# Kernel tuning notes

Measured on AMD Instinct MI355X. Metric: run time of the kernel, lower is better.

Reference implementation:

```python
import jax, jax.numpy as jnp
import numpy as np

B, T, C, L = 512, 256, 256, 64  # batch, time, num_classes (blank = C-1), max label len
NEG = -1e30  # log-space "zero"
EPS = 1e-7   # keras K.epsilon()


def setup_inputs() -> dict:
    key = jax.random.key(0)
    k1, k2, k3, k4 = jax.random.split(key, 4)
    # y_pred are post-softmax probabilities (output of the recognizer head)
    y_pred = jax.nn.softmax(jax.random.normal(k1, (B, T, C), jnp.float32), axis=-1)
    labels = jax.random.randint(k2, (B, L), 0, C - 1, dtype=jnp.int32)  # exclude blank
    input_length = jax.random.randint(k3, (B, 1), T // 2, T + 1, dtype=jnp.int32)
    label_length = jax.random.randint(k4, (B, 1), 16, 49, dtype=jnp.int32)
    return {"y_pred": y_pred, "labels": labels,
            "input_length": input_length, "label_length": label_length}


def _ctc_batch_cost(y_pred, labels, input_length, label_length):
    # Faithful to K.ctc_batch_cost: blank = num_classes-1, loss = -log p(labels | y_pred).
    Bn, Tn, Cn = y_pred.shape
    Ln = labels.shape[1]
    S = 2 * Ln + 1
    blank = Cn - 1
    log_probs = jnp.log(y_pred + EPS)                      # [B,T,C]

    # Extended label sequence: blank, l1, blank, l2, ..., blank  -> [B,S]
    ext = jnp.full((Bn, S), blank, dtype=labels.dtype)
    ext = ext.at[:, 1::2].set(labels)

    # Skip transition (s-2 -> s) allowed iff ext[s] != blank and ext[s] != ext[s-2]
    same2 = jnp.concatenate(
        [jnp.ones((Bn, 2), bool), ext[:, 2:] == ext[:, :-2]], axis=1)
    allow_skip = (ext != blank) & ~same2                   # [B,S]

    # Emission log-probs gathered along the extended sequence: [B,T,S]
    emit = jnp.take_along_axis(log_probs, jnp.broadcast_to(ext[:, None, :], (Bn, Tn, S)), axis=2)

    # alpha at t=0: can start at first blank or first label
    alpha0 = jnp.full((Bn, S), NEG, dtype=log_probs.dtype)
    alpha0 = alpha0.at[:, 0].set(emit[:, 0, 0])
    alpha0 = alpha0.at[:, 1].set(emit[:, 0, 1])

    def shift1(a):
        return jnp.concatenate([jnp.full((Bn, 1), NEG, a.dtype), a[:, :-1]], axis=1)

    def step(alpha, xs):
        emit_t, active = xs                                # [B,S], [B,1] bool
        a1 = shift1(alpha)
        a2 = shift1(a1)
        a2 = jnp.where(allow_skip, a2, NEG)
        new = jax.nn.logsumexp(jnp.stack([alpha, a1, a2]), axis=0) + emit_t
        new = jnp.where(active, new, alpha)                # freeze past input_length
        return new, None

    emits = jnp.transpose(emit, (1, 0, 2))[1:]             # [T-1,B,S]
    active = jnp.arange(1, Tn)[:, None, None] < input_length[None, :, :]  # [T-1,B,1]
    alpha_T, _ = jax.lax.scan(step, alpha0, (emits, active))

    # Terminal states: last label (s = 2*ll-1) or final blank (s = 2*ll)
    ll = label_length[:, 0]
    idx = jnp.stack([2 * ll - 1, 2 * ll], axis=1)          # [B,2]
    final = jnp.take_along_axis(alpha_T, idx, axis=1)
    return -jax.nn.logsumexp(final, axis=1, keepdims=True)  # [B,1]


def reference(y_pred, labels, input_length, label_length):
    return _ctc_batch_cost(y_pred, labels, input_length, label_length)
```

## Files before the change

### kernel.cpp

```cpp
#include <hip/hip_runtime.h>

#define TT 256
#define CC 256
#define LLAB 64
#define EPSF 1e-7f
#define CH 32
#define NSLOT 2
#define LN2F 0.69314718055994531f

__device__ __forceinline__ float wave_shr1_zero(float x) {
    int r = __builtin_amdgcn_update_dpp(0, __float_as_int(x), 0x138, 0xF, 0xF, false);
    return __int_as_float(r);
}

__device__ __forceinline__ float wave_max64(float x) {
#define DSTEP(ctrl)                                                            \
    { int t_ = __builtin_amdgcn_update_dpp(__float_as_int(x), __float_as_int(x),\
                                           (ctrl), 0xF, 0xF, false);           \
      x = fmaxf(x, __int_as_float(t_)); }
    DSTEP(0x111) DSTEP(0x112) DSTEP(0x114) DSTEP(0x118) DSTEP(0x142) DSTEP(0x143)
#undef DSTEP
    return __int_as_float(__builtin_amdgcn_readlane(__float_as_int(x), 63));
}

extern "C" __global__ __launch_bounds__(128) void ctc_fwd(
    const float* __restrict__ y_pred,
    const int* __restrict__ labels,
    const int* __restrict__ input_length,
    const int* __restrict__ label_length,
    float* __restrict__ out)
{
    const int b   = blockIdx.x;
    const int l   = threadIdx.x & 63;
    const int wid = threadIdx.x >> 6;

    __shared__ float lab_lds[NSLOT][CH][LLAB];
    __shared__ float blank_lds[NSLOT][CH];

    int len = input_length[b];
    len = len < 1 ? 1 : (len > TT ? TT : len);
    const int tmax = len - 1;
    const int nch  = (len - 1 + CH - 1) / CH;

    int llm = label_length[b];
    llm = llm < 1 ? 1 : (llm > LLAB ? LLAB : llm);

    const int  lab   = labels[b * LLAB + l];
    const bool ldlab = (l < llm);

    const float* __restrict__ yp = y_pred + (size_t)b * (TT * CC);
    const float* __restrict__ pl = yp + lab;
    const float* __restrict__ pb = yp + (CC - 1);

    float s0 = 0.f, s1 = 0.f, s2 = 0.f, skipf = 0.f;
    int   eacc = 0;

    float labA[CH], labB[CH], blA = 0.f, blB = 0.f;

#define ISSUE(c, labv, blv)                                                  \
    if ((c) < nch) {                                                         \
        const int t0 = 1 + (c) * CH;                                         \
        _Pragma("unroll")                                                    \
        for (int j = 0; j < CH; ++j) {                                       \
            int t = t0 + j; t = t > tmax ? tmax : t;                         \
            labv[j] = ldlab ? pl[t * CC] : 0.f;                              \
        }                                                                    \
        { int t = t0 + (l & (CH - 1)); t = t > tmax ? tmax : t;              \
          blv = pb[t * CC]; }                                                \
    }

#define FINISH(c, labv, blv)                                                 \
    if ((c) < nch) {                                                         \
        const int slot_ = (c) & (NSLOT - 1);                                 \
        if (l < CH) blank_lds[slot_][l] = blv + EPSF;                        \
        _Pragma("unroll")                                                    \
        for (int j = 0; j < CH; ++j)                                         \
            lab_lds[slot_][j][l] = ldlab ? (labv[j] + EPSF) : 0.f;           \
    }

    if (wid == 1) {
        ISSUE(0, labA, blA);
        ISSUE(1, labB, blB);
        FINISH(0, labA, blA);
    } else {
        const int labp = __shfl_up(lab, 1);
        skipf = (l >= 1 && lab != labp) ? 1.f : 0.f;
        if (l == 0) {
            s0 = pb[0] + EPSF;
            s1 = pl[0] + EPSF;
        }
    }
    __syncthreads();

    for (int k = 0; k < nch; ++k) {
        if (wid == 1) {
            if ((k & 1) == 0) { ISSUE(k + 2, labA, blA); FINISH(k + 1, labB, blB); }
            else              { ISSUE(k + 2, labB, blB); FINISH(k + 1, labA, blA); }
        } else {
            const int slot = k & (NSLOT - 1);
            float e[CH], bb[CH];
#pragma unroll
            for (int j = 0; j < CH; ++j) {
                e[j]  = lab_lds[slot][j][l];
                bb[j] = blank_lds[slot][j];
            }
#pragma unroll
            for (int j = 0; j < CH; ++j) {
                const int t = 1 + k * CH + j;
                float am1 = wave_shr1_zero(s1);
                float n0 = (s0 + am1) * bb[j];
                float n1 = fmaf(am1, skipf, s1 + s0) * e[j];
                float n2 = (s2 + s1) * bb[j];
                const bool act = t < len;
                s0 = act ? n0 : s0;
                s1 = act ? n1 : s1;
                s2 = act ? n2 : s2;
                if ((j & 3) == 3) {
                    float m = wave_max64(fmaxf(fmaxf(s0, s1), s2));
                    int me = __float_as_int(m) >> 23;
                    me = me < 26 ? 26 : me;
                    float scale = __int_as_float((253 - me) << 23);
                    s0 *= scale; s1 *= scale; s2 *= scale;
                    eacc += me - 126;
                }
            }
        }
        __syncthreads();
    }

    if (wid == 0) {
        float v1 = __shfl(s1, llm - 1);
        float v2 = (llm < LLAB) ? __shfl(s0, llm) : __shfl(s2, 63);
        float v  = fmaxf(v1 + v2, 1e-37f);
        if (l == 0) out[b] = -(__logf(v) + (float)eacc * LN2F);
    }
}

extern "C" void kernel_launch(void* const* d_in, const int* in_sizes, int n_in,
                              void* d_out, int out_size, void* d_ws, size_t ws_size,
                              hipStream_t stream) {
    (void)n_in; (void)out_size; (void)d_ws; (void)ws_size;
    const float* y_pred       = (const float*)d_in[0];
    const int*   labels       = (const int*)d_in[1];
    const int*   input_length = (const int*)d_in[2];
    const int*   label_length = (const int*)d_in[3];
    float* out = (float*)d_out;

    const int B = in_sizes[2];
    ctc_fwd<<<dim3(B), dim3(128), 0, stream>>>(y_pred, labels, input_length, label_length, out);
}
```

Measured before the change: 192.6 us.

## Load emissions directly into LDS via global_load_lds with manual vmcnt barriers

The producer wave now uses global_load_lds to stream the label and blank emission columns straight into a 4-slot LDS ring, instead of loading into registers and writing them to LDS. The EPS add and label masking move to the consumer wave. Each iteration waits with a hand-written vmcnt count and a raw s_barrier, replacing the two __syncthreads. This removes the register staging and the LDS store work from the producer and aims for deeper prefetch, but correctness depends on the hard-coded vmcnt(33) matching the 33 loads issued per chunk and on the slot reuse timing.

```diff
diff --git a/kernel.cpp b/kernel.cpp
--- a/kernel.cpp
+++ b/kernel.cpp
@@ -5,7 +5,7 @@
 #define LLAB 64
 #define EPSF 1e-7f
 #define CH 32
-#define NSLOT 2
+#define NSLOT 4
 #define LN2F 0.69314718055994531f
 
 __device__ __forceinline__ float wave_shr1_zero(float x) {
@@ -23,6 +23,12 @@
     return __int_as_float(__builtin_amdgcn_readlane(__float_as_int(x), 63));
 }
 
+__device__ __forceinline__ void gload_lds4(const float* g, float* lds) {
+    __builtin_amdgcn_global_load_lds(
+        (const __attribute__((address_space(1))) void*)g,
+        (__attribute__((address_space(3))) void*)lds, 4, 0, 0);
+}
+
 extern "C" __global__ __launch_bounds__(128) void ctc_fwd(
     const float* __restrict__ y_pred,
     const int* __restrict__ labels,
@@ -35,7 +41,7 @@
     const int wid = threadIdx.x >> 6;
 
     __shared__ float lab_lds[NSLOT][CH][LLAB];
-    __shared__ float blank_lds[NSLOT][CH];
+    __shared__ float blank_lds[NSLOT][LLAB];
 
     int len = input_length[b];
     len = len < 1 ? 1 : (len > TT ? TT : len);
@@ -51,37 +57,27 @@
     const float* __restrict__ yp = y_pred + (size_t)b * (TT * CC);
     const float* __restrict__ pl = yp + lab;
     const float* __restrict__ pb = yp + (CC - 1);
+    const float* __restrict__ psrc = ldlab ? pl : pb;
 
     float s0 = 0.f, s1 = 0.f, s2 = 0.f, skipf = 0.f;
     int   eacc = 0;
 
-    float labA[CH], labB[CH], blA = 0.f, blB = 0.f;
-
-#define ISSUE(c, labv, blv)                                                  \
+#define ISSUE_LDS(c)                                                         \
     if ((c) < nch) {                                                         \
+        const int slot_ = (c) & (NSLOT - 1);                                 \
         const int t0 = 1 + (c) * CH;                                         \
+        { int t = t0 + (l & (CH - 1)); t = t > tmax ? tmax : t;              \
+          gload_lds4(pb + t * CC, &blank_lds[slot_][0]); }                   \
         _Pragma("unroll")                                                    \
         for (int j = 0; j < CH; ++j) {                                       \
             int t = t0 + j; t = t > tmax ? tmax : t;                         \
-            labv[j] = ldlab ? pl[t * CC] : 0.f;                              \
+            gload_lds4(psrc + t * CC, &lab_lds[slot_][j][0]);                \
         }                                                                    \
-        { int t = t0 + (l & (CH - 1)); t = t > tmax ? tmax : t;              \
-          blv = pb[t * CC]; }                                                \
-    }
-
-#define FINISH(c, labv, blv)                                                 \
-    if ((c) < nch) {                                                         \
-        const int slot_ = (c) & (NSLOT - 1);                                 \
-        if (l < CH) blank_lds[slot_][l] = blv + EPSF;                        \
-        _Pragma("unroll")                                                    \
-        for (int j = 0; j < CH; ++j)                                         \
-            lab_lds[slot_][j][l] = ldlab ? (labv[j] + EPSF) : 0.f;           \
     }
 
     if (wid == 1) {
-        ISSUE(0, labA, blA);
-        ISSUE(1, labB, blB);
-        FINISH(0, labA, blA);
+        ISSUE_LDS(0);
+        ISSUE_LDS(1);
     } else {
         const int labp = __shfl_up(lab, 1);
         skipf = (l >= 1 && lab != labp) ? 1.f : 0.f;
@@ -90,19 +86,22 @@
             s1 = pl[0] + EPSF;
         }
     }
-    __syncthreads();
 
     for (int k = 0; k < nch; ++k) {
         if (wid == 1) {
-            if ((k & 1) == 0) { ISSUE(k + 2, labA, blA); FINISH(k + 1, labB, blB); }
-            else              { ISSUE(k + 2, labB, blB); FINISH(k + 1, labA, blA); }
+            if (k + 1 < nch) asm volatile("s_waitcnt vmcnt(33)" ::: "memory");
+            else             asm volatile("s_waitcnt vmcnt(0)"  ::: "memory");
+        }
+        asm volatile("s_barrier" ::: "memory");
+        if (wid == 1) {
+            ISSUE_LDS(k + 2);
         } else {
             const int slot = k & (NSLOT - 1);
             float e[CH], bb[CH];
 #pragma unroll
             for (int j = 0; j < CH; ++j) {
-                e[j]  = lab_lds[slot][j][l];
-                bb[j] = blank_lds[slot][j];
+                e[j]  = ldlab ? (lab_lds[slot][j][l] + EPSF) : 0.f;
+                bb[j] = blank_lds[slot][j] + EPSF;
             }
 #pragma unroll
             for (int j = 0; j < CH; ++j) {
@@ -125,7 +124,6 @@
                 }
             }
         }
-        __syncthreads();
     }
 
     if (wid == 0) {
```

Result: no change. 194.8 us (+1.2%).
